# Performance work log

Measured on AMD Instinct MI355X. Metric: run time of the kernel, lower is better.

## Reference

```python
import jax, jax.numpy as jnp
import numpy as np

H, DH = 8, 64  # num_heads, head_dim


def setup_inputs() -> dict:
    key = jax.random.key(0)
    ks = jax.random.split(key, 7)
    m, nq, nkv, d = 4, 2048, 2048, 512
    return {
        "xq": jax.random.normal(ks[0], (m, nq, d), jnp.float32),
        "xk": jax.random.normal(ks[1], (m, nkv, d), jnp.float32),
        "xv": jax.random.normal(ks[2], (m, nkv, d), jnp.float32),
        "Wq": jax.random.normal(ks[3], (d, H * DH), jnp.float32) * 0.02,
        "Wk": jax.random.normal(ks[4], (d, H * DH), jnp.float32) * 0.02,
        "Wv": jax.random.normal(ks[5], (d, H * DH), jnp.float32) * 0.02,
        "Wo": jax.random.normal(ks[6], (H * DH, d), jnp.float32) * 0.02,
        "bo": jnp.zeros((d,), jnp.float32),
    }


def _split_heads(t):
    # [b, n, h*d] -> [b, h, n, d]
    b, n, _ = t.shape
    return t.reshape(b, n, H, DH).transpose(0, 2, 1, 3)


def reference(xq, xk, xv, Wq, Wk, Wv, Wo, bo):
    scale = DH ** -0.5
    q = _split_heads(xq @ Wq)   # [b,h,nq,dh]
    k = _split_heads(xk @ Wk)   # [b,h,nkv,dh]
    v = _split_heads(xv @ Wv)   # [b,h,nkv,dh]
    dots = jnp.einsum("bhqd,bhkd->bhqk", q, k) * scale  # [b,h,nq,nkv]
    # diagonal attention term: query attends to its own (k,v) projection
    xq_k = _split_heads(xq @ Wk)
    xq_v = _split_heads(xq @ Wv)
    diag = jnp.sum(q * xq_k, axis=-1, keepdims=True) * scale  # [b,h,nq,1]
    dots = jnp.concatenate([dots, diag], axis=-1)  # [b,h,nq,nkv+1]
    attn = jax.nn.softmax(dots, axis=-1)
    out = jnp.einsum("bhqk,bhkd->bhqd", attn[..., :-1], v) + attn[..., -1:] * xq_v
    b, _, nq, _ = out.shape
    out = out.transpose(0, 2, 1, 3).reshape(b, nq, H * DH)  # merge heads
    return out @ Wo + bo
```

## Files before the change

### kernel.cpp

```cpp
#include <hip/hip_runtime.h>

#define LOG2E 1.44269504088896f
#define CS (0.125f * LOG2E)

typedef __bf16 bf16x8 __attribute__((ext_vector_type(8)));
typedef float f32x4 __attribute__((ext_vector_type(4)));
typedef unsigned short u16x8 __attribute__((ext_vector_type(8)));

__device__ __forceinline__ unsigned short f2bf(float f) {
  union { float f; unsigned int u; } v{f};
  unsigned int r = v.u + 0x7fffu + ((v.u >> 16) & 1u);
  return (unsigned short)(r >> 16);
}
__device__ __forceinline__ float bf2f(unsigned short u) {
  union { unsigned int u; float f; } v; v.u = ((unsigned int)u) << 16; return v.f;
}
__device__ __forceinline__ unsigned int pkr(float a, float b) {
  unsigned int ua = __builtin_bit_cast(unsigned int, a) + 0x8000u;
  unsigned int ub = __builtin_bit_cast(unsigned int, b) + 0x8000u;
  return __builtin_amdgcn_perm(ub, ua, 0x07060302);
}

typedef __attribute__((address_space(3))) unsigned int lds32_t;
typedef const __attribute__((address_space(1))) unsigned int glb32_t;
__device__ __forceinline__ void gld16(const unsigned short* g, unsigned short* l) {
  __builtin_amdgcn_global_load_lds((glb32_t*)(unsigned long long)g,
                                   (lds32_t*)(unsigned int)(unsigned long long)l,
                                   16, 0, 0);
}

__global__ __launch_bounds__(256) void conv_x(
    const float* __restrict__ xq, const float* __restrict__ xk, const float* __restrict__ xv,
    unsigned short* __restrict__ oq, unsigned short* __restrict__ ok, unsigned short* __restrict__ ov) {
  const int N4 = (8192 * 512) / 4;
  int idx = blockIdx.x * 256 + threadIdx.x;
  const float* src; unsigned short* dst; int i;
  if (idx < N4)          { src = xq; dst = oq; i = idx; }
  else if (idx < 2 * N4) { src = xk; dst = ok; i = idx - N4; }
  else                   { src = xv; dst = ov; i = idx - 2 * N4; }
  float4 v = ((const float4*)src)[i];
  ushort4 o; o.x = f2bf(v.x); o.y = f2bf(v.y); o.z = f2bf(v.z); o.w = f2bf(v.w);
  ((ushort4*)dst)[i] = o;
}

__global__ __launch_bounds__(256) void conv_w(
    const float* __restrict__ Wq, const float* __restrict__ Wk,
    const float* __restrict__ Wv, const float* __restrict__ Wo,
    unsigned short* __restrict__ oWq, unsigned short* __restrict__ oWk,
    unsigned short* __restrict__ oWv, unsigned short* __restrict__ oWo) {
  __shared__ unsigned short T[64 * 65];
  const int wsel = blockIdx.x >> 6;
  const int tile = blockIdx.x & 63;
  const int tk = (tile >> 3) * 64, tn = (tile & 7) * 64;
  const float* src = (wsel == 0) ? Wq : (wsel == 1) ? Wk : (wsel == 2) ? Wv : Wo;
  unsigned short* dst = (wsel == 0) ? oWq : (wsel == 1) ? oWk : (wsel == 2) ? oWv : oWo;
  const float scale = (wsel == 0) ? CS : 1.0f;
  const int rr = threadIdx.x >> 4;
  const int cc = (threadIdx.x & 15) * 4;
#pragma unroll
  for (int i = 0; i < 4; i++) {
    int row = rr + i * 16;
    float4 v = *(const float4*)&src[(size_t)(tk + row) * 512 + tn + cc];
    T[(cc + 0) * 65 + row] = f2bf(v.x * scale);
    T[(cc + 1) * 65 + row] = f2bf(v.y * scale);
    T[(cc + 2) * 65 + row] = f2bf(v.z * scale);
    T[(cc + 3) * 65 + row] = f2bf(v.w * scale);
  }
  __syncthreads();
#pragma unroll
  for (int i = 0; i < 4; i++) {
    int n = rr + i * 16;
    ushort4 o;
    o.x = T[n * 65 + cc + 0]; o.y = T[n * 65 + cc + 1];
    o.z = T[n * 65 + cc + 2]; o.w = T[n * 65 + cc + 3];
    *(ushort4*)&dst[(size_t)(tn + n) * 512 + tk + cc] = o;
  }
}

__device__ __forceinline__ void gemm_tile(
    const unsigned short* __restrict__ A, const unsigned short* __restrict__ Bt,
    int rowBlk, int colBlk, unsigned short* As, unsigned short* Bs, f32x4 (&acc)[4][4]) {
  const int t = threadIdx.x;
  const int lane = t & 63, c = lane & 15, g = lane >> 4;
  const int w = t >> 6;
  const int wm = w & 1, wn = w >> 1;
#pragma unroll
  for (int i = 0; i < 4; i++)
#pragma unroll
    for (int j = 0; j < 4; j++)
#pragma unroll
      for (int r = 0; r < 4; r++) acc[i][j][r] = 0.f;

  for (int kk = 0; kk < 512; kk += 32) {
    __syncthreads();
#pragma unroll
    for (int i = 0; i < 2; i++) {
      int idx = t + 256 * i;
      int r = idx >> 2, ch = idx & 3;
      gld16(&A[(size_t)(rowBlk + r) * 512 + kk + ch * 8], &As[idx * 8]);
      gld16(&Bt[(size_t)(colBlk + r) * 512 + kk + ch * 8], &Bs[idx * 8]);
    }
    __syncthreads();
    bf16x8 af[4], bfr[4];
#pragma unroll
    for (int i = 0; i < 4; i++)
      af[i] = __builtin_bit_cast(bf16x8, *(const u16x8*)&As[(wm * 64 + i * 16 + c) * 32 + g * 8]);
#pragma unroll
    for (int j = 0; j < 4; j++)
      bfr[j] = __builtin_bit_cast(bf16x8, *(const u16x8*)&Bs[(wn * 64 + j * 16 + c) * 32 + g * 8]);
#pragma unroll
    for (int i = 0; i < 4; i++)
#pragma unroll
      for (int j = 0; j < 4; j++)
        acc[i][j] = __builtin_amdgcn_mfma_f32_16x16x32_bf16(af[i], bfr[j], acc[i][j], 0, 0, 0);
  }
}

__global__ __launch_bounds__(256) void proj_all(
    const unsigned short* __restrict__ xq, const unsigned short* __restrict__ xk,
    const unsigned short* __restrict__ xv,
    const unsigned short* __restrict__ Wq, const unsigned short* __restrict__ Wk,
    const unsigned short* __restrict__ Wv,
    unsigned short* __restrict__ Qo, unsigned short* __restrict__ XKo,
    unsigned short* __restrict__ XVo, unsigned short* __restrict__ Ko,
    unsigned short* __restrict__ Vto) {
  __shared__ unsigned short As[128 * 32];
  __shared__ unsigned short Bs[128 * 32];
  const int rowBlk = blockIdx.x * 128;
  const int y = blockIdx.y;
  const unsigned short* A; const unsigned short* Bt; int colBlk; int mode;
  unsigned short* out;
  if (y < 12) {
    int wsel = y >> 2;
    A = xq; colBlk = (y & 3) * 128; mode = 0;
    Bt = (wsel == 0) ? Wq : (wsel == 1) ? Wk : Wv;
    out = (wsel == 0) ? Qo : (wsel == 1) ? XKo : XVo;
  } else if (y < 16) {
    A = xk; Bt = Wk; out = Ko; colBlk = (y - 12) * 128; mode = 0;
  } else {
    A = xv; Bt = Wv; out = Vto; colBlk = (y - 16) * 128; mode = 1;
  }
  f32x4 acc[4][4];
  gemm_tile(A, Bt, rowBlk, colBlk, As, Bs, acc);
  const int t = threadIdx.x;
  const int w = t >> 6, lane = t & 63, c = lane & 15, g = lane >> 4;
  const int wm = w & 1, wn = w >> 1;
  if (mode == 0) {
#pragma unroll
    for (int i = 0; i < 4; i++)
#pragma unroll
      for (int j = 0; j < 4; j++)
#pragma unroll
        for (int r = 0; r < 4; r++) {
          int row = rowBlk + wm * 64 + i * 16 + g * 4 + r;
          int col = colBlk + wn * 64 + j * 16 + c;
          out[(size_t)row * 512 + col] = f2bf(acc[i][j][r]);
        }
  } else {
#pragma unroll
    for (int i = 0; i < 4; i++)
#pragma unroll
      for (int j = 0; j < 4; j++)
#pragma unroll
        for (int r = 0; r < 4; r++) {
          int row = rowBlk + wm * 64 + i * 16 + g * 4 + r;
          int col = colBlk + wn * 64 + j * 16 + c;
          int bb = row >> 11, n = row & 2047;
          int hh = col >> 6, dh = col & 63;
          out[((size_t)(bb * 8 + hh) * 64 + dh) * 2048 + n] = f2bf(acc[i][j][r]);
        }
  }
}

__global__ __launch_bounds__(256) void gemm_out(
    const unsigned short* __restrict__ A, const unsigned short* __restrict__ Bt,
    float* __restrict__ out, const float* __restrict__ bias) {
  __shared__ unsigned short As[128 * 32];
  __shared__ unsigned short Bs[128 * 32];
  const int rowBlk = blockIdx.x * 128;
  const int colBlk = blockIdx.y * 128;
  f32x4 acc[4][4];
  gemm_tile(A, Bt, rowBlk, colBlk, As, Bs, acc);
  const int t = threadIdx.x;
  const int w = t >> 6, lane = t & 63, c = lane & 15, g = lane >> 4;
  const int wm = w & 1, wn = w >> 1;
#pragma unroll
  for (int i = 0; i < 4; i++)
#pragma unroll
    for (int j = 0; j < 4; j++)
#pragma unroll
      for (int r = 0; r < 4; r++) {
        int row = rowBlk + wm * 64 + i * 16 + g * 4 + r;
        int col = colBlk + wn * 64 + j * 16 + c;
        out[(size_t)row * 512 + col] = acc[i][j][r] + bias[col];
      }
}

__global__ __launch_bounds__(512, 8) void attn_kernel(
    const unsigned short* __restrict__ Q, const unsigned short* __restrict__ K,
    const unsigned short* __restrict__ Vt, const unsigned short* __restrict__ XK,
    const unsigned short* __restrict__ XV, unsigned short* __restrict__ O) {
  __shared__ unsigned short Ks[64 * 72];
  __shared__ unsigned short Vs[64 * 72];
  __shared__ unsigned short Ps[8][16 * 72];
  __shared__ float Scr[8][32];
  const int t = threadIdx.x;
  const int w = t >> 6, lane = t & 63, c = lane & 15, g = lane >> 4;
  const int qt = blockIdx.x, h = blockIdx.y, b = blockIdx.z;
  const size_t hb = (size_t)b * (2048 * 512) + h * 64;
  const size_t vhb = (size_t)(b * 8 + h) * 64 * 2048;
  const int qbase = qt * 128 + w * 16;
  unsigned short* Pw = &Ps[w][0];

  const int sr = t >> 3, sch = t & 7;
  const size_t kgoff = hb + (size_t)sr * 512 + sch * 8;
  const size_t vgoff = vhb + (size_t)sr * 2048 + sch * 8;
  const int soff = sr * 72 + sch * 8;

  bf16x8 qf[2];
#pragma unroll
  for (int hf = 0; hf < 2; hf++)
    qf[hf] = __builtin_bit_cast(bf16x8,
        *(const u16x8*)&Q[hb + (size_t)(qbase + c) * 512 + hf * 32 + g * 8]);

  f32x4 accO[4];
  float lq = 0.f;
#pragma unroll
  for (int jd = 0; jd < 4; jd++)
#pragma unroll
    for (int r = 0; r < 4; r++) accO[jd][r] = 0.f;

  u16x8 kreg = *(const u16x8*)&K[kgoff];
  u16x8 vreg = *(const u16x8*)&Vt[vgoff];
  *(u16x8*)&Ks[soff] = kreg;
  *(u16x8*)&Vs[soff] = vreg;
  __syncthreads();

  for (int kt = 0; kt < 32; kt++) {
    if (kt < 31) {
      kreg = *(const u16x8*)&K[kgoff + (size_t)(kt + 1) * 64 * 512];
      vreg = *(const u16x8*)&Vt[vgoff + (size_t)(kt + 1) * 64];
    }

    f32x4 s[4];
#pragma unroll
    for (int j = 0; j < 4; j++) {
      bf16x8 kf0 = __builtin_bit_cast(bf16x8, *(const u16x8*)&Ks[(j * 16 + c) * 72 + g * 8]);
      bf16x8 kf1 = __builtin_bit_cast(bf16x8, *(const u16x8*)&Ks[(j * 16 + c) * 72 + 32 + g * 8]);
      f32x4 z; z[0] = z[1] = z[2] = z[3] = 0.f;
      z = __builtin_amdgcn_mfma_f32_16x16x32_bf16(kf0, qf[0], z, 0, 0, 0);
      z = __builtin_amdgcn_mfma_f32_16x16x32_bf16(kf1, qf[1], z, 0, 0, 0);
      s[j] = z;
    }

    float sum = 0.f;
#pragma unroll
    for (int j = 0; j < 4; j++) {
      float p0 = exp2f(s[j][0]);
      float p1 = exp2f(s[j][1]);
      float p2 = exp2f(s[j][2]);
      float p3 = exp2f(s[j][3]);
      sum += (p0 + p1) + (p2 + p3);
      uint2 pw; pw.x = pkr(p0, p1); pw.y = pkr(p2, p3);
      *(uint2*)&Pw[c * 72 + j * 16 + g * 4] = pw;
    }
    lq += sum;

    bf16x8 pf0 = __builtin_bit_cast(bf16x8, *(const u16x8*)&Pw[c * 72 + g * 8]);
    bf16x8 pf1 = __builtin_bit_cast(bf16x8, *(const u16x8*)&Pw[c * 72 + 32 + g * 8]);
#pragma unroll
    for (int jd = 0; jd < 4; jd++) {
      bf16x8 v0 = __builtin_bit_cast(bf16x8, *(const u16x8*)&Vs[(jd * 16 + c) * 72 + g * 8]);
      bf16x8 v1 = __builtin_bit_cast(bf16x8, *(const u16x8*)&Vs[(jd * 16 + c) * 72 + 32 + g * 8]);
      accO[jd] = __builtin_amdgcn_mfma_f32_16x16x32_bf16(pf0, v0, accO[jd], 0, 0, 0);
      accO[jd] = __builtin_amdgcn_mfma_f32_16x16x32_bf16(pf1, v1, accO[jd], 0, 0, 0);
    }

    if (kt < 31) {
      __syncthreads();
      *(u16x8*)&Ks[soff] = kreg;
      *(u16x8*)&Vs[soff] = vreg;
      __syncthreads();
    }
  }

  lq += __shfl_xor(lq, 16);
  lq += __shfl_xor(lq, 32);

  {
    const int qc = qbase + c;
    float part = 0.f;
    {
      const unsigned short* qp = &Q[hb + (size_t)qc * 512 + g * 16];
      const unsigned short* xp = &XK[hb + (size_t)qc * 512 + g * 16];
      u16x8 q0 = *(const u16x8*)&qp[0], q1 = *(const u16x8*)&qp[8];
      u16x8 x0 = *(const u16x8*)&xp[0], x1 = *(const u16x8*)&xp[8];
#pragma unroll
      for (int ii = 0; ii < 8; ii++)
        part += bf2f(q0[ii]) * bf2f(x0[ii]) + bf2f(q1[ii]) * bf2f(x1[ii]);
    }
    part += __shfl_xor(part, 16);
    part += __shfl_xor(part, 32);
    float pd = exp2f(part);
    float inv = 1.f / (lq + pd);
    if (g == 0) {
      Scr[w][c] = inv;
      Scr[w][16 + c] = pd * inv;
    }
    __builtin_amdgcn_s_waitcnt(0);
    f32x4 a4 = *(const f32x4*)&Scr[w][g * 4];
    f32x4 p4 = *(const f32x4*)&Scr[w][16 + g * 4];
#pragma unroll
    for (int jd = 0; jd < 4; jd++)
#pragma unroll
      for (int r = 0; r < 4; r++) {
        int qr = qbase + g * 4 + r;
        float xv = bf2f(XV[hb + (size_t)qr * 512 + jd * 16 + c]);
        float val = accO[jd][r] * a4[r] + p4[r] * xv;
        O[((size_t)(b * 2048 + qr)) * 512 + h * 64 + jd * 16 + c] = f2bf(val);
      }
  }
}

extern "C" void kernel_launch(void* const* d_in, const int* in_sizes, int n_in,
                              void* d_out, int out_size, void* d_ws, size_t ws_size,
                              hipStream_t stream) {
  const float* xq = (const float*)d_in[0];
  const float* xk = (const float*)d_in[1];
  const float* xv = (const float*)d_in[2];
  const float* Wq = (const float*)d_in[3];
  const float* Wk = (const float*)d_in[4];
  const float* Wv = (const float*)d_in[5];
  const float* Wo = (const float*)d_in[6];
  const float* bo = (const float*)d_in[7];

  unsigned short* ws = (unsigned short*)d_ws;
  const size_t MD = 8192ull * 512;
  const size_t WD = 512ull * 512;
  unsigned short* xq_b = ws;
  unsigned short* xk_b = xq_b + MD;
  unsigned short* xv_b = xk_b + MD;
  unsigned short* Wq_t = xv_b + MD;
  unsigned short* Wk_t = Wq_t + WD;
  unsigned short* Wv_t = Wk_t + WD;
  unsigned short* Wo_t = Wv_t + WD;
  unsigned short* Qb  = Wo_t + WD;
  unsigned short* Kb  = Qb + MD;
  unsigned short* Vtb = Kb + MD;
  unsigned short* XKb = Vtb + MD;
  unsigned short* XVb = XKb + MD;
  unsigned short* Ob  = XVb + MD;

  conv_x<<<dim3(12288), 256, 0, stream>>>(xq, xk, xv, xq_b, xk_b, xv_b);
  conv_w<<<dim3(256), 256, 0, stream>>>(Wq, Wk, Wv, Wo, Wq_t, Wk_t, Wv_t, Wo_t);
  proj_all<<<dim3(64, 20), 256, 0, stream>>>(xq_b, xk_b, xv_b, Wq_t, Wk_t, Wv_t,
                                             Qb, XKb, XVb, Kb, Vtb);
  attn_kernel<<<dim3(16, 8, 4), 512, 0, stream>>>(Qb, Kb, Vtb, XKb, XVb, Ob);
  gemm_out<<<dim3(64, 4), 256, 0, stream>>>(Ob, Wo_t, (float*)d_out, bo);
}
```

Measured before the change: 229.3 us.

## Merge conversion kernels, halve gemm_out column tile, relax attention launch bounds

```diff
diff --git a/kernel.cpp b/kernel.cpp
--- a/kernel.cpp
+++ b/kernel.cpp
@@ -29,51 +29,53 @@
                                    16, 0, 0);
 }
 
-__global__ __launch_bounds__(256) void conv_x(
+__global__ __launch_bounds__(256) void conv_all(
     const float* __restrict__ xq, const float* __restrict__ xk, const float* __restrict__ xv,
-    unsigned short* __restrict__ oq, unsigned short* __restrict__ ok, unsigned short* __restrict__ ov) {
-  const int N4 = (8192 * 512) / 4;
-  int idx = blockIdx.x * 256 + threadIdx.x;
-  const float* src; unsigned short* dst; int i;
-  if (idx < N4)          { src = xq; dst = oq; i = idx; }
-  else if (idx < 2 * N4) { src = xk; dst = ok; i = idx - N4; }
-  else                   { src = xv; dst = ov; i = idx - 2 * N4; }
-  float4 v = ((const float4*)src)[i];
-  ushort4 o; o.x = f2bf(v.x); o.y = f2bf(v.y); o.z = f2bf(v.z); o.w = f2bf(v.w);
-  ((ushort4*)dst)[i] = o;
-}
-
-__global__ __launch_bounds__(256) void conv_w(
     const float* __restrict__ Wq, const float* __restrict__ Wk,
     const float* __restrict__ Wv, const float* __restrict__ Wo,
+    unsigned short* __restrict__ oxq, unsigned short* __restrict__ oxk, unsigned short* __restrict__ oxv,
     unsigned short* __restrict__ oWq, unsigned short* __restrict__ oWk,
     unsigned short* __restrict__ oWv, unsigned short* __restrict__ oWo) {
   __shared__ unsigned short T[64 * 65];
-  const int wsel = blockIdx.x >> 6;
-  const int tile = blockIdx.x & 63;
-  const int tk = (tile >> 3) * 64, tn = (tile & 7) * 64;
-  const float* src = (wsel == 0) ? Wq : (wsel == 1) ? Wk : (wsel == 2) ? Wv : Wo;
-  unsigned short* dst = (wsel == 0) ? oWq : (wsel == 1) ? oWk : (wsel == 2) ? oWv : oWo;
-  const float scale = (wsel == 0) ? CS : 1.0f;
-  const int rr = threadIdx.x >> 4;
-  const int cc = (threadIdx.x & 15) * 4;
-#pragma unroll
-  for (int i = 0; i < 4; i++) {
-    int row = rr + i * 16;
-    float4 v = *(const float4*)&src[(size_t)(tk + row) * 512 + tn + cc];
-    T[(cc + 0) * 65 + row] = f2bf(v.x * scale);
-    T[(cc + 1) * 65 + row] = f2bf(v.y * scale);
-    T[(cc + 2) * 65 + row] = f2bf(v.z * scale);
-    T[(cc + 3) * 65 + row] = f2bf(v.w * scale);
-  }
-  __syncthreads();
-#pragma unroll
-  for (int i = 0; i < 4; i++) {
-    int n = rr + i * 16;
-    ushort4 o;
-    o.x = T[n * 65 + cc + 0]; o.y = T[n * 65 + cc + 1];
-    o.z = T[n * 65 + cc + 2]; o.w = T[n * 65 + cc + 3];
-    *(ushort4*)&dst[(size_t)(tn + n) * 512 + tk + cc] = o;
+  const int blk = blockIdx.x;
+  if (blk < 12288) {
+    const int N4 = (8192 * 512) / 4;
+    int idx = blk * 256 + threadIdx.x;
+    const float* src; unsigned short* dst; int i;
+    if (idx < N4)          { src = xq; dst = oxq; i = idx; }
+    else if (idx < 2 * N4) { src = xk; dst = oxk; i = idx - N4; }
+    else                   { src = xv; dst = oxv; i = idx - 2 * N4; }
+    float4 v = ((const float4*)src)[i];
+    ushort4 o; o.x = f2bf(v.x); o.y = f2bf(v.y); o.z = f2bf(v.z); o.w = f2bf(v.w);
+    ((ushort4*)dst)[i] = o;
+  } else {
+    const int wblk = blk - 12288;
+    const int wsel = wblk >> 6;
+    const int tile = wblk & 63;
+    const int tk = (tile >> 3) * 64, tn = (tile & 7) * 64;
+    const float* src = (wsel == 0) ? Wq : (wsel == 1) ? Wk : (wsel == 2) ? Wv : Wo;
+    unsigned short* dst = (wsel == 0) ? oWq : (wsel == 1) ? oWk : (wsel == 2) ? oWv : oWo;
+    const float scale = (wsel == 0) ? CS : 1.0f;
+    const int rr = threadIdx.x >> 4;
+    const int cc = (threadIdx.x & 15) * 4;
+#pragma unroll
+    for (int i = 0; i < 4; i++) {
+      int row = rr + i * 16;
+      float4 v = *(const float4*)&src[(size_t)(tk + row) * 512 + tn + cc];
+      T[(cc + 0) * 65 + row] = f2bf(v.x * scale);
+      T[(cc + 1) * 65 + row] = f2bf(v.y * scale);
+      T[(cc + 2) * 65 + row] = f2bf(v.z * scale);
+      T[(cc + 3) * 65 + row] = f2bf(v.w * scale);
+    }
+    __syncthreads();
+#pragma unroll
+    for (int i = 0; i < 4; i++) {
+      int n = rr + i * 16;
+      ushort4 o;
+      o.x = T[n * 65 + cc + 0]; o.y = T[n * 65 + cc + 1];
+      o.z = T[n * 65 + cc + 2]; o.w = T[n * 65 + cc + 3];
+      *(ushort4*)&dst[(size_t)(tn + n) * 512 + tk + cc] = o;
+    }
   }
 }
 
@@ -176,27 +178,60 @@
     const unsigned short* __restrict__ A, const unsigned short* __restrict__ Bt,
     float* __restrict__ out, const float* __restrict__ bias) {
   __shared__ unsigned short As[128 * 32];
-  __shared__ unsigned short Bs[128 * 32];
+  __shared__ unsigned short Bs[64 * 32];
   const int rowBlk = blockIdx.x * 128;
-  const int colBlk = blockIdx.y * 128;
-  f32x4 acc[4][4];
-  gemm_tile(A, Bt, rowBlk, colBlk, As, Bs, acc);
+  const int colBlk = blockIdx.y * 64;
   const int t = threadIdx.x;
-  const int w = t >> 6, lane = t & 63, c = lane & 15, g = lane >> 4;
+  const int lane = t & 63, c = lane & 15, g = lane >> 4;
+  const int w = t >> 6;
   const int wm = w & 1, wn = w >> 1;
+  f32x4 acc[4][2];
 #pragma unroll
   for (int i = 0; i < 4; i++)
 #pragma unroll
-    for (int j = 0; j < 4; j++)
+    for (int j = 0; j < 2; j++)
+#pragma unroll
+      for (int r = 0; r < 4; r++) acc[i][j][r] = 0.f;
+
+  for (int kk = 0; kk < 512; kk += 32) {
+    __syncthreads();
+#pragma unroll
+    for (int i = 0; i < 2; i++) {
+      int idx = t + 256 * i;
+      int r = idx >> 2, ch = idx & 3;
+      gld16(&A[(size_t)(rowBlk + r) * 512 + kk + ch * 8], &As[idx * 8]);
+    }
+    {
+      int r = t >> 2, ch = t & 3;
+      gld16(&Bt[(size_t)(colBlk + r) * 512 + kk + ch * 8], &Bs[t * 8]);
+    }
+    __syncthreads();
+    bf16x8 af[4], bfr[2];
+#pragma unroll
+    for (int i = 0; i < 4; i++)
+      af[i] = __builtin_bit_cast(bf16x8, *(const u16x8*)&As[(wm * 64 + i * 16 + c) * 32 + g * 8]);
+#pragma unroll
+    for (int j = 0; j < 2; j++)
+      bfr[j] = __builtin_bit_cast(bf16x8, *(const u16x8*)&Bs[(wn * 32 + j * 16 + c) * 32 + g * 8]);
+#pragma unroll
+    for (int i = 0; i < 4; i++)
+#pragma unroll
+      for (int j = 0; j < 2; j++)
+        acc[i][j] = __builtin_amdgcn_mfma_f32_16x16x32_bf16(af[i], bfr[j], acc[i][j], 0, 0, 0);
+  }
+#pragma unroll
+  for (int i = 0; i < 4; i++)
+#pragma unroll
+    for (int j = 0; j < 2; j++)
 #pragma unroll
       for (int r = 0; r < 4; r++) {
         int row = rowBlk + wm * 64 + i * 16 + g * 4 + r;
-        int col = colBlk + wn * 64 + j * 16 + c;
+        int col = colBlk + wn * 32 + j * 16 + c;
         out[(size_t)row * 512 + col] = acc[i][j][r] + bias[col];
       }
 }
 
-__global__ __launch_bounds__(512, 8) void attn_kernel(
+__global__ __launch_bounds__(512, 4) void attn_kernel(
     const unsigned short* __restrict__ Q, const unsigned short* __restrict__ K,
     const unsigned short* __restrict__ Vt, const unsigned short* __restrict__ XK,
     const unsigned short* __restrict__ XV, unsigned short* __restrict__ O) {
@@ -351,10 +386,10 @@
   unsigned short* XVb = XKb + MD;
   unsigned short* Ob  = XVb + MD;
 
-  conv_x<<<dim3(12288), 256, 0, stream>>>(xq, xk, xv, xq_b, xk_b, xv_b);
-  conv_w<<<dim3(256), 256, 0, stream>>>(Wq, Wk, Wv, Wo, Wq_t, Wk_t, Wv_t, Wo_t);
+  conv_all<<<dim3(12544), 256, 0, stream>>>(xq, xk, xv, Wq, Wk, Wv, Wo,
+                                            xq_b, xk_b, xv_b, Wq_t, Wk_t, Wv_t, Wo_t);
   proj_all<<<dim3(64, 20), 256, 0, stream>>>(xq_b, xk_b, xv_b, Wq_t, Wk_t, Wv_t,
                                              Qb, XKb, XVb, Kb, Vtb);
   attn_kernel<<<dim3(16, 8, 4), 512, 0, stream>>>(Qb, Kb, Vtb, XKb, XVb, Ob);
-  gemm_out<<<dim3(64, 4), 256, 0, stream>>>(Ob, Wo_t, (float*)d_out, bo);
-}
+  gemm_out<<<dim3(64, 8), 256, 0, stream>>>(Ob, Wo_t, (float*)d_out, bo);
+}
```

Result: faster. 217.7 us (-5.0%).
